# Kernel optimization log

Measured on AMD Instinct MI355X. Metric: run time of the kernel, lower is better.

Reference implementation:

```python
import jax, jax.numpy as jnp
import numpy as np


def setup_inputs() -> dict:
    key = jax.random.key(0)
    k1, k2, k3, k4 = jax.random.split(key, 4)
    c = 256
    x = jax.random.normal(k1, (4, c, 64, 64), dtype=jnp.float32)
    # 1x1 conv weights act as channel-mixing matrices
    w_qkv = jax.random.normal(k2, (3 * c, c), dtype=jnp.float32) * (1.0 / np.sqrt(c))
    w_out = jax.random.normal(k3, (c, c), dtype=jnp.float32) * (1.0 / np.sqrt(c))
    b_out = jax.random.normal(k4, (c,), dtype=jnp.float32) * 0.01
    return {"x": x, "w_qkv": w_qkv, "w_out": w_out, "b_out": b_out}


def reference(x, w_qkv, w_out, b_out):
    b, c, h, w = x.shape
    heads = 4
    d = c // heads
    scale = d ** (-0.5)
    hw = h * w

    # 1x1 conv (no bias): [b,3c,h,w]
    qkv = jnp.einsum('oc,bchw->bohw', w_qkv, x)
    q, k, v = jnp.split(qkv, 3, axis=1)

    def to_seq(t):
        # [b,c,h,w] -> [b,heads,hw,d]
        return t.reshape(b, heads, d, hw).transpose(0, 1, 3, 2)

    q, k, v = to_seq(q), to_seq(k), to_seq(v)

    sim = jnp.einsum('bhid,bhjd->bhij', q, k) * scale
    attn = jax.nn.softmax(sim, axis=-1)
    out = jnp.einsum('bhij,bhjd->bhid', attn, v)

    # [b,heads,hw,d] -> [b,c,h,w]
    out = out.transpose(0, 1, 3, 2).reshape(b, c, h, w)

    # output 1x1 conv with bias, plus residual
    proj = jnp.einsum('oc,bchw->bohw', w_out, out) + b_out[None, :, None, None]
    return x + proj
```

## Files before the change

### kernel.cpp

```cpp
#include <hip/hip_runtime.h>


#define HW 4096
#define CIN 256
#define LOG2E_DIV8 0.18033688011112042f

typedef __attribute__((ext_vector_type(8))) short short8v;
typedef __attribute__((ext_vector_type(4))) short short4v;
typedef __attribute__((ext_vector_type(4))) float float4v;

static __device__ __forceinline__ unsigned short f2bf(float f) {
    unsigned int u = __float_as_uint(f);
    u += 0x7fff + ((u >> 16) & 1);
    return (unsigned short)(u >> 16);
}
static __device__ __forceinline__ unsigned int pkbf(float a, float b) {
    unsigned int r;
    asm("v_cvt_pk_bf16_f32 %0, %1, %2" : "=v"(r) : "v"(a), "v"(b));
    return r;
}

__global__ __launch_bounds__(256) void cast_w_k(
    const float* __restrict__ w_qkv, const float* __restrict__ w_out,
    unsigned short* __restrict__ wqb, unsigned short* __restrict__ wob)
{
    const int bi = blockIdx.x;
    if (bi < 192) {
        const int idx = bi * 1024 + threadIdx.x * 4;
        const float s = (idx < 256 * 256) ? LOG2E_DIV8 : 1.0f;
        const float4 v = *(const float4*)&w_qkv[idx];
        uint2 pk;
        pk.x = pkbf(v.x * s, v.y * s);
        pk.y = pkbf(v.z * s, v.w * s);
        *(uint2*)&wqb[idx] = pk;
    } else {
        const int idx = (bi - 192) * 1024 + threadIdx.x * 4;
        const float4 v = *(const float4*)&w_out[idx];
        uint2 pk;
        pk.x = pkbf(v.x, v.y);
        pk.y = pkbf(v.z, v.w);
        *(uint2*)&wob[idx] = pk;
    }
}

__global__ __launch_bounds__(256) void cast_x_k(
    const float* __restrict__ x, unsigned short* __restrict__ xt)
{
    const int p0 = blockIdx.x * 64, c0 = blockIdx.y * 64, b = blockIdx.z;
    const int t = threadIdx.x;
    __shared__ float tile[64][65];

    const float* xb = x + ((size_t)b * CIN + c0) * HW + p0;
    #pragma unroll
    for (int iter = 0; iter < 4; ++iter) {
        const int idx = iter * 1024 + t * 4;
        const int cc = idx >> 6, pp = idx & 63;
        const float4 v = *(const float4*)&xb[(size_t)cc * HW + pp];
        tile[cc][pp + 0] = v.x; tile[cc][pp + 1] = v.y;
        tile[cc][pp + 2] = v.z; tile[cc][pp + 3] = v.w;
    }
    __syncthreads();
    unsigned short* xo = xt + ((size_t)b * HW + p0) * CIN + c0;
    #pragma unroll
    for (int iter = 0; iter < 4; ++iter) {
        const int idx = iter * 1024 + t * 4;
        const int pp = idx >> 6, cc = idx & 63;
        uint2 pk;
        pk.x = pkbf(tile[cc + 0][pp], tile[cc + 1][pp]);
        pk.y = pkbf(tile[cc + 2][pp], tile[cc + 3][pp]);
        *(uint2*)&xo[(size_t)pp * CIN + cc] = pk;
    }
}

__global__ __launch_bounds__(256) void qkv_mfma_k(
    const unsigned short* __restrict__ wqb, const unsigned short* __restrict__ xt,
    unsigned short* __restrict__ qb, unsigned short* __restrict__ kb,
    unsigned short* __restrict__ vb)
{
    const int o0 = blockIdx.x * 128;
    const int p0 = blockIdx.y * 128;
    const int b  = blockIdx.z;
    const int t = threadIdx.x;
    const int wid = t >> 6, lane = t & 63, g = lane >> 4, li = lane & 15;
    const int wo = (wid >> 1) * 64, wp = (wid & 1) * 64;

    __shared__ char alds[16384];
    __shared__ char blds[16384];

    const int srow8 = t >> 3, sc16 = t & 7;
    const char* asrc = (const char*)wqb + ((size_t)(o0 + srow8) * 256) * 2 + sc16 * 16;
    const char* bsrc = (const char*)xt + (((size_t)b * HW + p0 + srow8) * 256) * 2 + sc16 * 16;

    float4 areg[4], breg[4];
    #pragma unroll
    for (int it = 0; it < 4; ++it) {
        areg[it] = *(const float4*)(asrc + (size_t)it * 32 * 512);
        breg[it] = *(const float4*)(bsrc + (size_t)it * 32 * 512);
    }

    float4v acc[4][4];
    #pragma unroll
    for (int mt = 0; mt < 4; ++mt)
        #pragma unroll
        for (int nt = 0; nt < 4; ++nt) acc[mt][nt] = (float4v){0.f, 0.f, 0.f, 0.f};

    for (int ks = 0; ks < 4; ++ks) {
        #pragma unroll
        for (int it = 0; it < 4; ++it) {
            const int row = it * 32 + srow8;
            const int dsw = row * 128 + ((sc16 * 16) ^ ((row & 7) << 4));
            *(float4*)(alds + dsw) = areg[it];
            *(float4*)(blds + dsw) = breg[it];
        }
        __syncthreads();
        if (ks < 3) {
            #pragma unroll
            for (int it = 0; it < 4; ++it) {
                areg[it] = *(const float4*)(asrc + (size_t)it * 32 * 512 + (ks + 1) * 128);
                breg[it] = *(const float4*)(bsrc + (size_t)it * 32 * 512 + (ks + 1) * 128);
            }
        }
        short8v af[4][2], bf[4][2];
        #pragma unroll
        for (int mt = 0; mt < 4; ++mt) {
            const int row = wo + mt * 16 + li;
            #pragma unroll
            for (int kc = 0; kc < 2; ++kc)
                af[mt][kc] = *(const short8v*)(alds + row * 128 + ((kc * 64 + g * 16) ^ ((row & 7) << 4)));
        }
        #pragma unroll
        for (int nt = 0; nt < 4; ++nt) {
            const int row = wp + nt * 16 + li;
            #pragma unroll
            for (int kc = 0; kc < 2; ++kc)
                bf[nt][kc] = *(const short8v*)(blds + row * 128 + ((kc * 64 + g * 16) ^ ((row & 7) << 4)));
        }
        #pragma unroll
        for (int mt = 0; mt < 4; ++mt)
            #pragma unroll
            for (int nt = 0; nt < 4; ++nt) {
                acc[mt][nt] = __builtin_amdgcn_mfma_f32_16x16x32_bf16(af[mt][0], bf[nt][0], acc[mt][nt], 0, 0, 0);
                acc[mt][nt] = __builtin_amdgcn_mfma_f32_16x16x32_bf16(af[mt][1], bf[nt][1], acc[mt][nt], 0, 0, 0);
            }
        __syncthreads();
    }

    const int which = o0 >> 8;
    #pragma unroll
    for (int mt = 0; mt < 4; ++mt) {
        const int o_b = o0 + wo + mt * 16 + g * 4;
        const int head = (o_b >> 6) & 3;
        const int dd = o_b & 63;
        const int bh = b * 4 + head;
        if (which < 2) {
            unsigned short* dst = which ? kb : qb;
            #pragma unroll
            for (int nt = 0; nt < 4; ++nt) {
                const int p = p0 + wp + nt * 16 + li;
                uint2 pk;
                pk.x = pkbf(acc[mt][nt][0], acc[mt][nt][1]);
                pk.y = pkbf(acc[mt][nt][2], acc[mt][nt][3]);
                *(uint2*)&dst[((size_t)bh * HW + p) * 64 + dd] = pk;
            }
        } else {
            #pragma unroll
            for (int nt = 0; nt < 4; ++nt) {
                const int p = p0 + wp + nt * 16 + li;
                #pragma unroll
                for (int r = 0; r < 4; ++r)
                    vb[((size_t)bh * 64 + dd + r) * HW + p] = f2bf(acc[mt][nt][r]);
            }
        }
    }
}

__global__ __launch_bounds__(256) void flash_mfma_k(
    const unsigned short* __restrict__ qb, const unsigned short* __restrict__ kb,
    const unsigned short* __restrict__ vb, unsigned short* __restrict__ att)
{
    const int i0 = blockIdx.x * 128;
    const int bh = blockIdx.y;
    const int t = threadIdx.x;
    const int wid = t >> 6, lane = t & 63, g = lane >> 4, li = lane & 15;
    const int b = bh >> 2, head = bh & 3;

    const unsigned short* qg = qb + (size_t)bh * HW * 64;
    const unsigned short* kg = kb + (size_t)bh * HW * 64;
    const unsigned short* vg = vb + (size_t)bh * 64 * HW;

    __shared__ char klds[2][8192];
    __shared__ char vlds[2][8192];
    __shared__ short plds[4][32][72];

    short8v qf[2][2];
    #pragma unroll
    for (int qt = 0; qt < 2; ++qt)
        #pragma unroll
        for (int c = 0; c < 2; ++c) {
            const int q = i0 + wid * 32 + qt * 16 + li;
            qf[qt][c] = *(const short8v*)(qg + (size_t)q * 64 + c * 32 + g * 8);
        }

    short8v ones;
    #pragma unroll
    for (int i = 0; i < 8; ++i) ones[i] = (short)0x3F80;

    float m[2] = {0.f, 0.f};
    float4v acco[4][2];
    float4v accl[2];
    float4v accs[4][2];
    #pragma unroll
    for (int dt = 0; dt < 4; ++dt)
        #pragma unroll
        for (int qt = 0; qt < 2; ++qt) acco[dt][qt] = (float4v){0.f, 0.f, 0.f, 0.f};
    accl[0] = (float4v){0.f, 0.f, 0.f, 0.f};
    accl[1] = (float4v){0.f, 0.f, 0.f, 0.f};

    const int srow0 = t >> 3, sc0 = t & 7;
    const int srow1 = (t + 256) >> 3;
    const int dsw0 = srow0 * 128 + ((sc0 * 16) ^ ((srow0 & 7) << 4));
    const int dsw1 = srow1 * 128 + ((sc0 * 16) ^ ((srow1 & 7) << 4));
    const char* ksrc0 = (const char*)kg + (size_t)srow0 * 128 + sc0 * 16;
    const char* ksrc1 = (const char*)kg + (size_t)srow1 * 128 + sc0 * 16;
    const char* vsrc0 = (const char*)vg + (size_t)srow0 * 8192 + sc0 * 16;
    const char* vsrc1 = (const char*)vg + (size_t)srow1 * 8192 + sc0 * 16;

    float4 kregA, kregB, vregA, vregB;

    auto LOADT = [&](int tile) {
        kregA = *(const float4*)(ksrc0 + (size_t)tile * 8192);
        kregB = *(const float4*)(ksrc1 + (size_t)tile * 8192);
        vregA = *(const float4*)(vsrc0 + (size_t)tile * 128);
        vregB = *(const float4*)(vsrc1 + (size_t)tile * 128);
    };
    auto WRITET = [&](int buf) {
        *(float4*)(klds[buf] + dsw0) = kregA;
        *(float4*)(klds[buf] + dsw1) = kregB;
        *(float4*)(vlds[buf] + dsw0) = vregA;
        *(float4*)(vlds[buf] + dsw1) = vregB;
    };
    auto SMM = [&](int buf) {
        #pragma unroll
        for (int jt = 0; jt < 4; ++jt) {
            accs[jt][0] = (float4v){-m[0], -m[0], -m[0], -m[0]};
            accs[jt][1] = (float4v){-m[1], -m[1], -m[1], -m[1]};
        }
        __builtin_amdgcn_s_setprio(1);
        #pragma unroll
        for (int jt = 0; jt < 4; ++jt) {
            const int row = jt * 16 + li;
            #pragma unroll
            for (int c = 0; c < 2; ++c) {
                const short8v kf = *(const short8v*)(klds[buf] + row * 128 + ((c * 64 + g * 16) ^ ((row & 7) << 4)));
                accs[jt][0] = __builtin_amdgcn_mfma_f32_16x16x32_bf16(kf, qf[0][c], accs[jt][0], 0, 0, 0);
                accs[jt][1] = __builtin_amdgcn_mfma_f32_16x16x32_bf16(kf, qf[1][c], accs[jt][1], 0, 0, 0);
            }
        }
        __builtin_amdgcn_s_setprio(0);
    };
    auto SOFT = [&]() {
        float tadj[2];
        #pragma unroll
        for (int qt = 0; qt < 2; ++qt) {
            float t0 = fmaxf(fmaxf(accs[0][qt][0], accs[0][qt][1]), fmaxf(accs[0][qt][2], accs[0][qt][3]));
            float t1 = fmaxf(fmaxf(accs[1][qt][0], accs[1][qt][1]), fmaxf(accs[1][qt][2], accs[1][qt][3]));
            float t2 = fmaxf(fmaxf(accs[2][qt][0], accs[2][qt][1]), fmaxf(accs[2][qt][2], accs[2][qt][3]));
            float t3 = fmaxf(fmaxf(accs[3][qt][0], accs[3][qt][1]), fmaxf(accs[3][qt][2], accs[3][qt][3]));
            float tm = fmaxf(fmaxf(t0, t1), fmaxf(t2, t3));
            tm = fmaxf(tm, __shfl_xor(tm, 16, 64));
            tm = fmaxf(tm, __shfl_xor(tm, 32, 64));
            tadj[qt] = tm;
        }
        if (__any(fmaxf(tadj[0], tadj[1]) > 8.0f)) {
            #pragma unroll
            for (int qt = 0; qt < 2; ++qt) {
                const float delta = fmaxf(tadj[qt], 0.f);
                const float fsc = __builtin_amdgcn_exp2f(-delta);
                m[qt] += delta;
                #pragma unroll
                for (int dt = 0; dt < 4; ++dt) {
                    acco[dt][qt][0] *= fsc; acco[dt][qt][1] *= fsc;
                    acco[dt][qt][2] *= fsc; acco[dt][qt][3] *= fsc;
                }
                accl[qt][0] *= fsc; accl[qt][1] *= fsc;
                accl[qt][2] *= fsc; accl[qt][3] *= fsc;
                #pragma unroll
                for (int jt = 0; jt < 4; ++jt) {
                    accs[jt][qt][0] -= delta; accs[jt][qt][1] -= delta;
                    accs[jt][qt][2] -= delta; accs[jt][qt][3] -= delta;
                }
            }
        }
        #pragma unroll
        for (int qt = 0; qt < 2; ++qt) {
            #pragma unroll
            for (int jt = 0; jt < 4; ++jt) {
                const float p0 = __builtin_amdgcn_exp2f(accs[jt][qt][0]);
                const float p1 = __builtin_amdgcn_exp2f(accs[jt][qt][1]);
                const float p2 = __builtin_amdgcn_exp2f(accs[jt][qt][2]);
                const float p3 = __builtin_amdgcn_exp2f(accs[jt][qt][3]);
                uint2 pk;
                pk.x = pkbf(p0, p1);
                pk.y = pkbf(p2, p3);
                *(uint2*)&plds[wid][qt * 16 + li][jt * 16 + 4 * g] = pk;
            }
        }
    };
    auto PVMM = [&](int buf) {
        short8v pf[2][2];
        #pragma unroll
        for (int qt = 0; qt < 2; ++qt)
            #pragma unroll
            for (int c = 0; c < 2; ++c)
                pf[qt][c] = *(const short8v*)((const char*)&plds[wid][qt * 16 + li][0] + c * 64 + g * 16);
        __builtin_amdgcn_s_setprio(1);
        #pragma unroll
        for (int qt = 0; qt < 2; ++qt) {
            accl[qt] = __builtin_amdgcn_mfma_f32_16x16x32_bf16(ones, pf[qt][0], accl[qt], 0, 0, 0);
            accl[qt] = __builtin_amdgcn_mfma_f32_16x16x32_bf16(ones, pf[qt][1], accl[qt], 0, 0, 0);
        }
        #pragma unroll
        for (int dt = 0; dt < 4; ++dt) {
            const int row = dt * 16 + li;
            #pragma unroll
            for (int c = 0; c < 2; ++c) {
                const short8v vf = *(const short8v*)(vlds[buf] + row * 128 + ((c * 64 + g * 16) ^ ((row & 7) << 4)));
                acco[dt][0] = __builtin_amdgcn_mfma_f32_16x16x32_bf16(vf, pf[0][c], acco[dt][0], 0, 0, 0);
                acco[dt][1] = __builtin_amdgcn_mfma_f32_16x16x32_bf16(vf, pf[1][c], acco[dt][1], 0, 0, 0);
            }
        }
        __builtin_amdgcn_s_setprio(0);
    };

    LOADT(0);
    WRITET(0);
    LOADT(1);
    __syncthreads();
    SMM(0);

    for (int kt = 0; kt < 63; ++kt) {
        const int nb = (kt + 1) & 1;
        WRITET(nb);
        const int pref = (kt + 2 < 64) ? kt + 2 : 63;
        LOADT(pref);
        SOFT();
        PVMM(kt & 1);
        __syncthreads();
        SMM(nb);
    }
    SOFT();
    PVMM(1);

    #pragma unroll
    for (int qt = 0; qt < 2; ++qt) {
        const float inv = 1.0f / accl[qt][0];
        const int q = i0 + wid * 32 + qt * 16 + li;
        #pragma unroll
        for (int dt = 0; dt < 4; ++dt) {
            uint2 pk;
            pk.x = pkbf(acco[dt][qt][0] * inv, acco[dt][qt][1] * inv);
            pk.y = pkbf(acco[dt][qt][2] * inv, acco[dt][qt][3] * inv);
            *(uint2*)&att[((size_t)b * HW + q) * CIN + head * 64 + dt * 16 + 4 * g] = pk;
        }
    }
}

__global__ __launch_bounds__(256) void proj_mfma_k(
    const unsigned short* __restrict__ wob, const unsigned short* __restrict__ att,
    const float* __restrict__ bias, const float* __restrict__ x,
    float* __restrict__ out)
{
    const int o0 = blockIdx.x * 128;
    const int p0 = blockIdx.y * 128;
    const int b  = blockIdx.z;
    const int t = threadIdx.x;
    const int wid = t >> 6, lane = t & 63, g = lane >> 4, li = lane & 15;
    const int wo = (wid >> 1) * 64, wp = (wid & 1) * 64;

    __shared__ char alds[16384];
    __shared__ char blds[16384];

    const int srow8 = t >> 3, sc16 = t & 7;
    const char* asrc = (const char*)wob + ((size_t)(o0 + srow8) * 256) * 2 + sc16 * 16;
    const char* bsrc = (const char*)att + (((size_t)b * HW + p0 + srow8) * 256) * 2 + sc16 * 16;

    float4 areg[4], breg[4];
    #pragma unroll
    for (int it = 0; it < 4; ++it) {
        areg[it] = *(const float4*)(asrc + (size_t)it * 32 * 512);
        breg[it] = *(const float4*)(bsrc + (size_t)it * 32 * 512);
    }

    float4v acc[4][4];
    #pragma unroll
    for (int mt = 0; mt < 4; ++mt)
        #pragma unroll
        for (int nt = 0; nt < 4; ++nt) acc[mt][nt] = (float4v){0.f, 0.f, 0.f, 0.f};

    for (int ks = 0; ks < 4; ++ks) {
        #pragma unroll
        for (int it = 0; it < 4; ++it) {
            const int row = it * 32 + srow8;
            const int dsw = row * 128 + ((sc16 * 16) ^ ((row & 7) << 4));
            *(float4*)(alds + dsw) = areg[it];
            *(float4*)(blds + dsw) = breg[it];
        }
        __syncthreads();
        if (ks < 3) {
            #pragma unroll
            for (int it = 0; it < 4; ++it) {
                areg[it] = *(const float4*)(asrc + (size_t)it * 32 * 512 + (ks + 1) * 128);
                breg[it] = *(const float4*)(bsrc + (size_t)it * 32 * 512 + (ks + 1) * 128);
            }
        }
        short8v af[4][2], bf[4][2];
        #pragma unroll
        for (int mt = 0; mt < 4; ++mt) {
            const int row = wo + mt * 16 + li;
            #pragma unroll
            for (int kc = 0; kc < 2; ++kc)
                af[mt][kc] = *(const short8v*)(alds + row * 128 + ((kc * 64 + g * 16) ^ ((row & 7) << 4)));
        }
        #pragma unroll
        for (int nt = 0; nt < 4; ++nt) {
            const int row = wp + nt * 16 + li;
            #pragma unroll
            for (int kc = 0; kc < 2; ++kc)
                bf[nt][kc] = *(const short8v*)(blds + row * 128 + ((kc * 64 + g * 16) ^ ((row & 7) << 4)));
        }
        #pragma unroll
        for (int mt = 0; mt < 4; ++mt)
            #pragma unroll
            for (int nt = 0; nt < 4; ++nt) {
                acc[mt][nt] = __builtin_amdgcn_mfma_f32_16x16x32_bf16(af[mt][0], bf[nt][0], acc[mt][nt], 0, 0, 0);
                acc[mt][nt] = __builtin_amdgcn_mfma_f32_16x16x32_bf16(af[mt][1], bf[nt][1], acc[mt][nt], 0, 0, 0);
            }
        __syncthreads();
    }

    #pragma unroll
    for (int mt = 0; mt < 4; ++mt) {
        const int o_b = o0 + wo + mt * 16 + g * 4;
        #pragma unroll
        for (int nt = 0; nt < 4; ++nt) {
            const int p = p0 + wp + nt * 16 + li;
            #pragma unroll
            for (int r = 0; r < 4; ++r) {
                const int o = o_b + r;
                const size_t ix = ((size_t)b * CIN + o) * HW + p;
                out[ix] = acc[mt][nt][r] + bias[o] + x[ix];
            }
        }
    }
}

extern "C" void kernel_launch(void* const* d_in, const int* in_sizes, int n_in,
                              void* d_out, int out_size, void* d_ws, size_t ws_size,
                              hipStream_t stream)
{
    const float* x     = (const float*)d_in[0];
    const float* w_qkv = (const float*)d_in[1];
    const float* w_out = (const float*)d_in[2];
    const float* b_out = (const float*)d_in[3];
    float* out = (float*)d_out;

    char* ws = (char*)d_ws;
    const size_t MB = 1024 * 1024;
    unsigned short* xt  = (unsigned short*)(ws);
    unsigned short* qb  = (unsigned short*)(ws + 8 * MB);
    unsigned short* kb  = (unsigned short*)(ws + 16 * MB);
    unsigned short* vb  = (unsigned short*)(ws + 24 * MB);
    unsigned short* att = (unsigned short*)(ws + 32 * MB);
    unsigned short* wqb = (unsigned short*)(ws + 40 * MB);
    unsigned short* wob = (unsigned short*)(ws + 40 * MB + 768 * 256 * 2);

    cast_w_k<<<256, 256, 0, stream>>>(w_qkv, w_out, wqb, wob);
    cast_x_k<<<dim3(64, 4, 4), 256, 0, stream>>>(x, xt);
    qkv_mfma_k<<<dim3(6, 32, 4), 256, 0, stream>>>(wqb, xt, qb, kb, vb);
    flash_mfma_k<<<dim3(32, 16), 256, 0, stream>>>(qb, kb, vb, att);
    proj_mfma_k<<<dim3(2, 32, 4), 256, 0, stream>>>(wob, att, b_out, x, out);
}
```

Before: 164.5 us.

## Switch flash attention to 32x32x16 MFMA and keep P in registers

```diff
diff --git a/kernel.cpp b/kernel.cpp
--- a/kernel.cpp
+++ b/kernel.cpp
@@ -8,6 +8,8 @@
 typedef __attribute__((ext_vector_type(8))) short short8v;
 typedef __attribute__((ext_vector_type(4))) short short4v;
 typedef __attribute__((ext_vector_type(4))) float float4v;
+typedef __attribute__((ext_vector_type(16))) float f32x16;
+typedef __attribute__((ext_vector_type(4))) unsigned int uint4v;
 
 static __device__ __forceinline__ unsigned short f2bf(float f) {
     unsigned int u = __float_as_uint(f);
@@ -18,6 +20,9 @@
     unsigned int r;
     asm("v_cvt_pk_bf16_f32 %0, %1, %2" : "=v"(r) : "v"(a), "v"(b));
     return r;
+}
+static __device__ __forceinline__ void pl32swap(unsigned int& a, unsigned int& b) {
+    asm volatile("v_permlane32_swap_b32 %0, %1" : "+v"(a), "+v"(b));
 }
 
 __global__ __launch_bounds__(256) void cast_w_k(
@@ -181,7 +186,8 @@
     const int i0 = blockIdx.x * 128;
     const int bh = blockIdx.y;
     const int t = threadIdx.x;
-    const int wid = t >> 6, lane = t & 63, g = lane >> 4, li = lane & 15;
+    const int wid = t >> 6, lane = t & 63;
+    const int q32 = lane & 31, hi = lane >> 5;
     const int b = bh >> 2, head = bh & 3;
 
     const unsigned short* qg = qb + (size_t)bh * HW * 64;
@@ -190,34 +196,27 @@
 
     __shared__ char klds[2][8192];
     __shared__ char vlds[2][8192];
-    __shared__ short plds[4][32][72];
-
-    short8v qf[2][2];
-    #pragma unroll
-    for (int qt = 0; qt < 2; ++qt)
-        #pragma unroll
-        for (int c = 0; c < 2; ++c) {
-            const int q = i0 + wid * 32 + qt * 16 + li;
-            qf[qt][c] = *(const short8v*)(qg + (size_t)q * 64 + c * 32 + g * 8);
-        }
+
+    const int q = i0 + wid * 32 + q32;
+    short8v qf[4];
+    #pragma unroll
+    for (int kc = 0; kc < 4; ++kc)
+        qf[kc] = *(const short8v*)(qg + (size_t)q * 64 + kc * 16 + hi * 8);
 
     short8v ones;
     #pragma unroll
     for (int i = 0; i < 8; ++i) ones[i] = (short)0x3F80;
 
-    float m[2] = {0.f, 0.f};
-    float4v acco[4][2];
-    float4v accl[2];
-    float4v accs[4][2];
-    #pragma unroll
-    for (int dt = 0; dt < 4; ++dt)
-        #pragma unroll
-        for (int qt = 0; qt < 2; ++qt) acco[dt][qt] = (float4v){0.f, 0.f, 0.f, 0.f};
-    accl[0] = (float4v){0.f, 0.f, 0.f, 0.f};
-    accl[1] = (float4v){0.f, 0.f, 0.f, 0.f};
+    float m = 0.f;
+    f32x16 acco[2];
+    f32x16 accl;
+    f32x16 accs[2];
+    short8v pf[2][2];
+    #pragma unroll
+    for (int r = 0; r < 16; ++r) { acco[0][r] = 0.f; acco[1][r] = 0.f; accl[r] = 0.f; }
 
     const int srow0 = t >> 3, sc0 = t & 7;
-    const int srow1 = (t + 256) >> 3;
+    const int srow1 = srow0 + 32;
     const int dsw0 = srow0 * 128 + ((sc0 * 16) ^ ((srow0 & 7) << 4));
     const int dsw1 = srow1 * 128 + ((sc0 * 16) ^ ((srow1 & 7) << 4));
     const char* ksrc0 = (const char*)kg + (size_t)srow0 * 128 + sc0 * 16;
@@ -241,93 +240,82 @@
     };
     auto SMM = [&](int buf) {
         #pragma unroll
-        for (int jt = 0; jt < 4; ++jt) {
-            accs[jt][0] = (float4v){-m[0], -m[0], -m[0], -m[0]};
-            accs[jt][1] = (float4v){-m[1], -m[1], -m[1], -m[1]};
-        }
+        for (int r = 0; r < 16; ++r) { accs[0][r] = -m; accs[1][r] = -m; }
         __builtin_amdgcn_s_setprio(1);
         #pragma unroll
-        for (int jt = 0; jt < 4; ++jt) {
-            const int row = jt * 16 + li;
-            #pragma unroll
-            for (int c = 0; c < 2; ++c) {
-                const short8v kf = *(const short8v*)(klds[buf] + row * 128 + ((c * 64 + g * 16) ^ ((row & 7) << 4)));
-                accs[jt][0] = __builtin_amdgcn_mfma_f32_16x16x32_bf16(kf, qf[0][c], accs[jt][0], 0, 0, 0);
-                accs[jt][1] = __builtin_amdgcn_mfma_f32_16x16x32_bf16(kf, qf[1][c], accs[jt][1], 0, 0, 0);
+        for (int jt = 0; jt < 2; ++jt) {
+            const int row = jt * 32 + q32;
+            const char* kbase = klds[buf] + row * 128;
+            const int sw = (row & 7) << 4;
+            #pragma unroll
+            for (int kc = 0; kc < 4; ++kc) {
+                const short8v kf = *(const short8v*)(kbase + ((kc * 32 + hi * 16) ^ sw));
+                accs[jt] = __builtin_amdgcn_mfma_f32_32x32x16_bf16(kf, qf[kc], accs[jt], 0, 0, 0);
             }
         }
         __builtin_amdgcn_s_setprio(0);
     };
     auto SOFT = [&]() {
-        float tadj[2];
-        #pragma unroll
-        for (int qt = 0; qt < 2; ++qt) {
-            float t0 = fmaxf(fmaxf(accs[0][qt][0], accs[0][qt][1]), fmaxf(accs[0][qt][2], accs[0][qt][3]));
-            float t1 = fmaxf(fmaxf(accs[1][qt][0], accs[1][qt][1]), fmaxf(accs[1][qt][2], accs[1][qt][3]));
-            float t2 = fmaxf(fmaxf(accs[2][qt][0], accs[2][qt][1]), fmaxf(accs[2][qt][2], accs[2][qt][3]));
-            float t3 = fmaxf(fmaxf(accs[3][qt][0], accs[3][qt][1]), fmaxf(accs[3][qt][2], accs[3][qt][3]));
-            float tm = fmaxf(fmaxf(t0, t1), fmaxf(t2, t3));
-            tm = fmaxf(tm, __shfl_xor(tm, 16, 64));
-            tm = fmaxf(tm, __shfl_xor(tm, 32, 64));
-            tadj[qt] = tm;
-        }
-        if (__any(fmaxf(tadj[0], tadj[1]) > 8.0f)) {
-            #pragma unroll
-            for (int qt = 0; qt < 2; ++qt) {
-                const float delta = fmaxf(tadj[qt], 0.f);
-                const float fsc = __builtin_amdgcn_exp2f(-delta);
-                m[qt] += delta;
-                #pragma unroll
-                for (int dt = 0; dt < 4; ++dt) {
-                    acco[dt][qt][0] *= fsc; acco[dt][qt][1] *= fsc;
-                    acco[dt][qt][2] *= fsc; acco[dt][qt][3] *= fsc;
-                }
-                accl[qt][0] *= fsc; accl[qt][1] *= fsc;
-                accl[qt][2] *= fsc; accl[qt][3] *= fsc;
-                #pragma unroll
-                for (int jt = 0; jt < 4; ++jt) {
-                    accs[jt][qt][0] -= delta; accs[jt][qt][1] -= delta;
-                    accs[jt][qt][2] -= delta; accs[jt][qt][3] -= delta;
-                }
-            }
-        }
-        #pragma unroll
-        for (int qt = 0; qt < 2; ++qt) {
-            #pragma unroll
-            for (int jt = 0; jt < 4; ++jt) {
-                const float p0 = __builtin_amdgcn_exp2f(accs[jt][qt][0]);
-                const float p1 = __builtin_amdgcn_exp2f(accs[jt][qt][1]);
-                const float p2 = __builtin_amdgcn_exp2f(accs[jt][qt][2]);
-                const float p3 = __builtin_amdgcn_exp2f(accs[jt][qt][3]);
-                uint2 pk;
-                pk.x = pkbf(p0, p1);
-                pk.y = pkbf(p2, p3);
-                *(uint2*)&plds[wid][qt * 16 + li][jt * 16 + 4 * g] = pk;
-            }
+        float mx[16];
+        #pragma unroll
+        for (int r = 0; r < 16; ++r) mx[r] = fmaxf(accs[0][r], accs[1][r]);
+        #pragma unroll
+        for (int s = 8; s > 0; s >>= 1)
+            #pragma unroll
+            for (int r = 0; r < s; ++r) mx[r] = fmaxf(mx[r], mx[r + s]);
+        const float tm = fmaxf(mx[0], __shfl_xor(mx[0], 32, 64));
+        if (__any(tm > 8.0f)) {
+            const float delta = fmaxf(tm, 0.f);
+            const float fsc = __builtin_amdgcn_exp2f(-delta);
+            m += delta;
+            accl[0] *= fsc;
+            #pragma unroll
+            for (int r = 0; r < 16; ++r) { acco[0][r] *= fsc; acco[1][r] *= fsc; }
+            #pragma unroll
+            for (int r = 0; r < 16; ++r) { accs[0][r] -= delta; accs[1][r] -= delta; }
+        }
+        #pragma unroll
+        for (int jt = 0; jt < 2; ++jt) {
+            float p[16];
+            #pragma unroll
+            for (int r = 0; r < 16; ++r) p[r] = __builtin_amdgcn_exp2f(accs[jt][r]);
+            unsigned int w0 = pkbf(p[0], p[1]);
+            unsigned int w1 = pkbf(p[2], p[3]);
+            unsigned int w2 = pkbf(p[4], p[5]);
+            unsigned int w3 = pkbf(p[6], p[7]);
+            pl32swap(w0, w2);
+            pl32swap(w1, w3);
+            uint4v fa; fa[0] = w0; fa[1] = w1; fa[2] = w2; fa[3] = w3;
+            pf[jt][0] = __builtin_bit_cast(short8v, fa);
+            unsigned int w4 = pkbf(p[8],  p[9]);
+            unsigned int w5 = pkbf(p[10], p[11]);
+            unsigned int w6 = pkbf(p[12], p[13]);
+            unsigned int w7 = pkbf(p[14], p[15]);
+            pl32swap(w4, w6);
+            pl32swap(w5, w7);
+            uint4v fb; fb[0] = w4; fb[1] = w5; fb[2] = w6; fb[3] = w7;
+            pf[jt][1] = __builtin_bit_cast(short8v, fb);
         }
     };
     auto PVMM = [&](int buf) {
-        short8v pf[2][2];
-        #pragma unroll
-        for (int qt = 0; qt < 2; ++qt)
-            #pragma unroll
-            for (int c = 0; c < 2; ++c)
-                pf[qt][c] = *(const short8v*)((const char*)&plds[wid][qt * 16 + li][0] + c * 64 + g * 16);
         __builtin_amdgcn_s_setprio(1);
         #pragma unroll
-        for (int qt = 0; qt < 2; ++qt) {
-            accl[qt] = __builtin_amdgcn_mfma_f32_16x16x32_bf16(ones, pf[qt][0], accl[qt], 0, 0, 0);
-            accl[qt] = __builtin_amdgcn_mfma_f32_16x16x32_bf16(ones, pf[qt][1], accl[qt], 0, 0, 0);
-        }
-        #pragma unroll
-        for (int dt = 0; dt < 4; ++dt) {
-            const int row = dt * 16 + li;
-            #pragma unroll
-            for (int c = 0; c < 2; ++c) {
-                const short8v vf = *(const short8v*)(vlds[buf] + row * 128 + ((c * 64 + g * 16) ^ ((row & 7) << 4)));
-                acco[dt][0] = __builtin_amdgcn_mfma_f32_16x16x32_bf16(vf, pf[0][c], acco[dt][0], 0, 0, 0);
-                acco[dt][1] = __builtin_amdgcn_mfma_f32_16x16x32_bf16(vf, pf[1][c], acco[dt][1], 0, 0, 0);
-            }
+        for (int jt = 0; jt < 2; ++jt)
+            #pragma unroll
+            for (int kr = 0; kr < 2; ++kr)
+                accl = __builtin_amdgcn_mfma_f32_32x32x16_bf16(ones, pf[jt][kr], accl, 0, 0, 0);
+        #pragma unroll
+        for (int dt = 0; dt < 2; ++dt) {
+            const int row = dt * 32 + q32;
+            const char* vbase = vlds[buf] + row * 128;
+            const int sw = (row & 7) << 4;
+            #pragma unroll
+            for (int jt = 0; jt < 2; ++jt)
+                #pragma unroll
+                for (int kr = 0; kr < 2; ++kr) {
+                    const short8v vf = *(const short8v*)(vbase + ((jt * 64 + kr * 32 + hi * 16) ^ sw));
+                    acco[dt] = __builtin_amdgcn_mfma_f32_32x32x16_bf16(vf, pf[jt][kr], acco[dt], 0, 0, 0);
+                }
         }
         __builtin_amdgcn_s_setprio(0);
     };
@@ -351,18 +339,18 @@
     SOFT();
     PVMM(1);
 
-    #pragma unroll
-    for (int qt = 0; qt < 2; ++qt) {
-        const float inv = 1.0f / accl[qt][0];
-        const int q = i0 + wid * 32 + qt * 16 + li;
-        #pragma unroll
-        for (int dt = 0; dt < 4; ++dt) {
+    const float inv = 1.0f / accl[0];
+    unsigned short* ao = att + ((size_t)b * HW + q) * CIN + head * 64;
+    #pragma unroll
+    for (int dt = 0; dt < 2; ++dt)
+        #pragma unroll
+        for (int g4 = 0; g4 < 4; ++g4) {
+            const int d = dt * 32 + 8 * g4 + 4 * hi;
             uint2 pk;
-            pk.x = pkbf(acco[dt][qt][0] * inv, acco[dt][qt][1] * inv);
-            pk.y = pkbf(acco[dt][qt][2] * inv, acco[dt][qt][3] * inv);
-            *(uint2*)&att[((size_t)b * HW + q) * CIN + head * 64 + dt * 16 + 4 * g] = pk;
-        }
-    }
+            pk.x = pkbf(acco[dt][g4 * 4 + 0] * inv, acco[dt][g4 * 4 + 1] * inv);
+            pk.y = pkbf(acco[dt][g4 * 4 + 2] * inv, acco[dt][g4 * 4 + 3] * inv);
+            *(uint2*)&ao[d] = pk;
+        }
 }
 
 __global__ __launch_bounds__(256) void proj_mfma_k(
```

After: 162.7 us. No clear change (-1.1%).
